# Kernel optimization log

Measured on AMD Instinct MI355X. Metric: run time of the kernel, lower is better.

The kernel has to match this reference:

```python
import jax, jax.numpy as jnp
import numpy as np

C = 3          # num_classes
A = 3          # num_anchors per cell
IMG = 1024.0
W_LOC, W_OBJ, W_CLS = 2.0, 1.0, 1.0
POS_T, NEG_T, HNM_RATIO = 0.5, 0.3, 3


def _make_anchors(H, W, stride):
    ys = (np.arange(H) + 0.5) * stride
    xs = (np.arange(W) + 0.5) * stride
    cy, cx = np.meshgrid(ys, xs, indexing='ij')
    sizes = np.array([2.0, 3.0, 4.0]) * stride          # A anchor scales
    cx = cx[:, :, None]; cy = cy[:, :, None]; s = sizes[None, None, :]
    a = np.stack([cx - s / 2, cy - s / 2, cx + s / 2, cy + s / 2], axis=-1)  # [H,W,A,4]
    return jnp.asarray(a.reshape(-1, 4), dtype=jnp.float32)


def setup_inputs() -> dict:
    key = jax.random.key(0)
    k1, k2, k3, k4, k5, k6 = jax.random.split(key, 6)
    B, M = 32, 20
    p1 = jax.random.normal(k1, (B, A * (5 + C), 128, 128), jnp.float32)
    p2 = jax.random.normal(k2, (B, A * (5 + C), 64, 64), jnp.float32)
    p3 = jax.random.normal(k3, (B, A * (5 + C), 32, 32), jnp.float32)
    anchors1 = _make_anchors(128, 128, 8)
    anchors2 = _make_anchors(64, 64, 16)
    anchors3 = _make_anchors(32, 32, 32)
    cxy = jax.random.uniform(k4, (B, M, 2), minval=0.0, maxval=IMG)
    wh = jax.random.uniform(k5, (B, M, 2), minval=16.0, maxval=256.0)
    boxes = jnp.clip(jnp.concatenate([cxy - wh / 2, cxy + wh / 2], -1), 0.0, IMG)
    labels = jax.random.randint(k6, (B, M), 0, C + 1)  # 0 = padding, 1..C = class
    return {"p1": p1, "p2": p2, "p3": p3,
            "anchors1": anchors1, "anchors2": anchors2, "anchors3": anchors3,
            "boxes": boxes, "labels": labels}


def _iou(anchors, boxes):
    # anchors [N,4], boxes [M,4], xyxy -> [N,M]
    lt = jnp.maximum(anchors[:, None, :2], boxes[None, :, :2])
    rb = jnp.minimum(anchors[:, None, 2:], boxes[None, :, 2:])
    wh = jnp.maximum(rb - lt, 0.0)
    inter = wh[..., 0] * wh[..., 1]
    area_a = (anchors[:, 2] - anchors[:, 0]) * (anchors[:, 3] - anchors[:, 1])
    area_b = (boxes[:, 2] - boxes[:, 0]) * (boxes[:, 3] - boxes[:, 1])
    return inter / jnp.maximum(area_a[:, None] + area_b[None, :] - inter, 1e-9)


def _decode(pred):
    # yolo_decode: [B, A*(5+C), H, W] -> deltas [B,N,4], obj [B,N], cls [B,N,C]; N = H*W*A
    B, _, H, W = pred.shape
    p = pred.reshape(B, A, 5 + C, H, W).transpose(0, 3, 4, 1, 2).reshape(B, H * W * A, 5 + C)
    return p[..., :4], p[..., 4], p[..., 5:]


def _level_loss(deltas, obj_logits, cls_logits, anchors, boxes, labels):
    # single image, single level
    valid = (labels > 0)
    iou = _iou(anchors, boxes) * valid[None, :].astype(deltas.dtype)
    best_iou = iou.max(axis=1)
    best_idx = iou.argmax(axis=1)
    pos = best_iou >= POS_T
    neg = best_iou < NEG_T
    mboxes = boxes[best_idx]
    mlabels = labels[best_idx]
    posf = pos.astype(deltas.dtype)
    # SmoothL1 (beta=1), mean over 4 coords, summed over positives
    d = jnp.abs(deltas - mboxes)
    sl1 = jnp.where(d < 1.0, 0.5 * d * d, d - 0.5).mean(axis=-1)
    loc = jnp.sum(sl1 * posf)
    # BCEWithLogits against objectness targets (= pos mask)
    x = obj_logits
    bce = jnp.maximum(x, 0.0) - x * posf + jnp.log1p(jnp.exp(-jnp.abs(x)))
    # hard negative mining on detached obj loss
    num_pos = pos.sum()
    num_neg = neg.sum()
    k = jnp.where(num_pos == 0,
                  jnp.minimum(100, num_neg),
                  jnp.minimum(num_pos * HNM_RATIO, num_neg))
    masked = jnp.where(neg, jax.lax.stop_gradient(bce), -1e9)
    order = jnp.argsort(-masked)
    ranks = jnp.zeros_like(order).at[order].set(jnp.arange(order.shape[0]))
    sel = (ranks < k) & neg
    obj = jnp.sum(bce * (pos | sel).astype(bce.dtype))
    # CrossEntropy over positives, labels shifted by -1
    logp = jax.nn.log_softmax(cls_logits, axis=-1)
    tgt = jnp.clip(mlabels - 1, 0, C - 1)
    nll = -jnp.take_along_axis(logp, tgt[:, None], axis=1)[:, 0]
    cls = jnp.sum(nll * posf)
    return loc, obj, cls, num_pos, sel.sum()


def reference(p1, p2, p3, anchors1, anchors2, anchors3, boxes, labels):
    total_loc = total_obj = total_cls = 0.0
    total_pos = total_neg = 0
    for pred, anchors in ((p1, anchors1), (p2, anchors2), (p3, anchors3)):
        deltas, obj_l, cls_l = _decode(pred)
        loc, obj, cls, npos, nneg = jax.vmap(
            _level_loss, in_axes=(0, 0, 0, None, 0, 0)
        )(deltas, obj_l, cls_l, anchors, boxes, labels)
        total_loc = total_loc + loc.sum()
        total_obj = total_obj + obj.sum()
        total_cls = total_cls + cls.sum()
        total_pos = total_pos + npos.sum()
        total_neg = total_neg + nneg.sum()
    norm = jnp.maximum(total_pos + total_neg, 1).astype(jnp.float32)
    loss_loc = W_LOC * total_loc / norm
    loss_obj = W_OBJ * total_obj / norm
    loss_cls = W_CLS * total_cls / jnp.maximum(total_pos, 1).astype(jnp.float32)
    return loss_loc + loss_obj + loss_cls, loss_loc, loss_obj, loss_cls
```

## Files before the change

### kernel.cpp

```cpp
#include <hip/hip_runtime.h>

#define NB 32
#define NM 20
#define NA 3
#define NCH 8
#define N0 49152
#define N1 12288
#define N2 3072


__device__ __forceinline__ float wredf(float v) {
  #pragma unroll
  for (int o = 32; o; o >>= 1) v += __shfl_down(v, o, 64);
  return v;
}

__device__ __forceinline__ float softplus_neg_abs(float x) {
  return __logf(1.0f + __expf(-fabsf(x)));
}

__device__ __forceinline__ float blockredf(float v, float* swred, int tid) {
  v = wredf(v);
  if ((tid & 63) == 0) swred[tid >> 6] = v;
  __syncthreads();
  float s = 0.f;
  if (tid == 0) {
    #pragma unroll
    for (int i = 0; i < 16; ++i) s += swred[i];
  }
  __syncthreads();
  return s;
}

__device__ __forceinline__ unsigned suffix1024(unsigned* scan, int tid) {
  #pragma unroll
  for (int d = 1; d < 1024; d <<= 1) {
    unsigned t = (tid + d < 1024) ? scan[tid + d] : 0u;
    __syncthreads();
    scan[tid] += t;
    __syncthreads();
  }
  return scan[tid];
}

__global__ __launch_bounds__(256, 8) void kA(
    const float* __restrict__ pr0, const float* __restrict__ pr1,
    const float* __restrict__ pr2,
    const float* __restrict__ boxes, const int* __restrict__ labels,
    unsigned* __restrict__ keys, float* __restrict__ partials)
{
  const int bx = blockIdx.x, b = blockIdx.y, tid = threadIdx.x;
  int blk, wshift, HW, nblk, koff, poff; float stride; const float* pred;
  if (bx < 64)      { blk = bx;      wshift = 7; HW = 16384; nblk = 64; koff = 0;            poff = 0;                         stride = 8.f;  pred = pr0; }
  else if (bx < 80) { blk = bx - 64; wshift = 6; HW = 4096;  nblk = 16; koff = NB * N0;      poff = NB * 64 * 5;               stride = 16.f; pred = pr1; }
  else              { blk = bx - 80; wshift = 5; HW = 1024;  nblk = 4;  koff = NB * (N0+N1); poff = NB * 64 * 5 + NB * 16 * 5; stride = 32.f; pred = pr2; }

  const int   nrows = 256 >> wshift;
  const int   h0    = blk * nrows;
  const float ymin  = ((float)h0 + 0.5f) * stride - 2.f * stride;
  const float ymax  = ((float)(h0 + nrows - 1) + 0.5f) * stride + 2.f * stride;

  __shared__ float4 sb4[NM + 1];
  __shared__ float2 sa2[NM + 1];
  __shared__ int    slab[NM + 1];
  __shared__ int    s_nv;
  if (tid < 64) {
    float x1 = 0, y1 = 0, x2 = 0, y2 = 0; int lb = 0; bool v = false;
    if (tid < NM) {
      x1 = boxes[(b * NM + tid) * 4 + 0];
      y1 = boxes[(b * NM + tid) * 4 + 1];
      x2 = boxes[(b * NM + tid) * 4 + 2];
      y2 = boxes[(b * NM + tid) * 4 + 3];
      lb = labels[b * NM + tid];
      v  = (lb > 0) && (y2 > ymin) && (y1 < ymax);
    }
    unsigned long long mask = __ballot(v);
    int pref = __popcll(mask & ((1ull << tid) - 1ull));
    if (v) {
      sb4[pref] = make_float4(x1, y1, x2, y2);
      sa2[pref] = make_float2((x2 - x1) * (y2 - y1), 0.f);
      slab[pref] = lb;
    }
    if (tid == 0) {
      int nv = (int)__popcll(mask);
      s_nv = nv;
      sb4[nv] = make_float4(0.f, 0.f, 0.f, 0.f);
      sa2[nv] = make_float2(0.f, 0.f);
    }
  }
  __syncthreads();

  const int hw = blk * 256 + tid;
  const int W  = 1 << wshift;
  const int w  = hw & (W - 1);
  const int h  = hw >> wshift;
  const float cx = ((float)w + 0.5f) * stride;
  const float cy = ((float)h + 0.5f) * stride;
  const float* pb = pred + (size_t)b * (NA * NCH) * HW + hw;

  float xo[NA];
  #pragma unroll
  for (int a = 0; a < NA; ++a) xo[a] = pb[(a * NCH + 4) * HW];

  float ax1[NA], ay1[NA], ax2[NA], ay2[NA], aar[NA];
  #pragma unroll
  for (int a = 0; a < NA; ++a) {
    const float s  = (2.0f + (float)a) * stride;
    const float hx = 0.5f * s;
    ax1[a] = cx - hx; ax2[a] = cx + hx;
    ay1[a] = cy - hx; ay2[a] = cy + hx;
    aar[a] = s * s;
  }

  float bi[NA] = {0.f, 0.f, 0.f};
  float bu[NA] = {1.f, 1.f, 1.f};
  int   bm[NA] = {0, 0, 0};
  const int nv = s_nv;

  float4 bb = sb4[0];
  float2 aa = sa2[0];
  for (int m = 0; m < nv; ++m) {
    const float4 nb = sb4[m + 1];
    const float2 na = sa2[m + 1];
    #pragma unroll
    for (int a = 0; a < NA; ++a) {
      float ix = fminf(ax2[a], bb.z) - fmaxf(ax1[a], bb.x);
      float iy = fminf(ay2[a], bb.w) - fmaxf(ay1[a], bb.y);
      float inter = fmaxf(ix, 0.f) * fmaxf(iy, 0.f);
      float un = (aar[a] + aa.x) - inter;
      bool better = inter * bu[a] > bi[a] * un;
      if (better) { bi[a] = inter; bu[a] = un; bm[a] = m; }
    }
    bb = nb; aa = na;
  }

  float loc_s = 0.f, obj_s = 0.f, cls_s = 0.f;
  float pos_c = 0.f, neg_c = 0.f;

  #pragma unroll
  for (int a = 0; a < NA; ++a) {
    const bool pos = 2.f * bi[a] >= bu[a];
    const bool neg = bi[a] < 0.3f * bu[a];
    const float x  = xo[a];
    const float sp = softplus_neg_abs(x);

    unsigned key = 0u;
    if (pos) {
      const int m = bm[a];
      pos_c += 1.f;
      obj_s += fmaxf(x, 0.f) - x + sp;
      const float4 tb = sb4[m];
      float ls = 0.f;
      float d0 = fabsf(pb[(a * NCH + 0) * HW] - tb.x);
      float d1 = fabsf(pb[(a * NCH + 1) * HW] - tb.y);
      float d2 = fabsf(pb[(a * NCH + 2) * HW] - tb.z);
      float d3 = fabsf(pb[(a * NCH + 3) * HW] - tb.w);
      ls += (d0 < 1.f) ? 0.5f * d0 * d0 : (d0 - 0.5f);
      ls += (d1 < 1.f) ? 0.5f * d1 * d1 : (d1 - 0.5f);
      ls += (d2 < 1.f) ? 0.5f * d2 * d2 : (d2 - 0.5f);
      ls += (d3 < 1.f) ? 0.5f * d3 * d3 : (d3 - 0.5f);
      loc_s += 0.25f * ls;
      float l0 = pb[(a * NCH + 5) * HW];
      float l1 = pb[(a * NCH + 6) * HW];
      float l2 = pb[(a * NCH + 7) * HW];
      float mx  = fmaxf(fmaxf(l0, l1), l2);
      float lse = mx + __logf(__expf(l0 - mx) + __expf(l1 - mx) + __expf(l2 - mx));
      int tgt = slab[m] - 1; tgt = tgt < 0 ? 0 : (tgt > 2 ? 2 : tgt);
      float lt = (tgt == 0) ? l0 : ((tgt == 1) ? l1 : l2);
      cls_s += lse - lt;
    } else if (neg) {
      neg_c += 1.f;
      float bn = fmaxf(x, 0.f) + sp;
      key = __float_as_uint(bn) | 0x80000000u;
    }
    keys[koff + b * (HW * NA) + a * HW + hw] = key;
  }

  loc_s = wredf(loc_s); obj_s = wredf(obj_s); cls_s = wredf(cls_s);
  pos_c = wredf(pos_c); neg_c = wredf(neg_c);
  __shared__ float sred[4][5];
  const int wv = tid >> 6;
  if ((tid & 63) == 0) {
    sred[wv][0] = loc_s; sred[wv][1] = obj_s; sred[wv][2] = cls_s;
    sred[wv][3] = pos_c; sred[wv][4] = neg_c;
  }
  __syncthreads();
  if (tid == 0) {
    float* slot = partials + poff + (size_t)(b * nblk + blk) * 5;
    #pragma unroll
    for (int j = 0; j < 5; ++j)
      slot[j] = sred[0][j] + sred[1][j] + sred[2][j] + sred[3][j];
  }
}

template<int NL4, bool GUARD>
__device__ float kb_core(const unsigned* __restrict__ kp, int n4, unsigned k,
                         unsigned* hist, unsigned* scan, float* fsum,
                         float* swred, unsigned* sh_sel, unsigned* sh_r, int tid)
{
  const uint4* kp4 = (const uint4*)kp;
  uint4 v[NL4];

  for (int i = tid; i < 4096; i += 1024) hist[i] = 0u;
  __syncthreads();

  #pragma unroll
  for (int j = 0; j < NL4; ++j)
    if (!GUARD || tid + j * 1024 < n4) v[j] = kp4[tid + j * 1024];

  #pragma unroll
  for (int j = 0; j < NL4; ++j)
    if (!GUARD || tid + j * 1024 < n4) {
      atomicAdd(&hist[v[j].x >> 20], 1u);
      atomicAdd(&hist[v[j].y >> 20], 1u);
      atomicAdd(&hist[v[j].z >> 20], 1u);
      atomicAdd(&hist[v[j].w >> 20], 1u);
    }
  __syncthreads();

  unsigned c0 = hist[tid*4], c1 = hist[tid*4+1], c2 = hist[tid*4+2], c3 = hist[tid*4+3];
  unsigned st = c0 + c1 + c2 + c3;
  scan[tid] = st;
  __syncthreads();
  unsigned I = suffix1024(scan, tid);
  unsigned H = I - st;
  if (H < k && k <= I) {
    unsigned cum = H;
    if (cum + c3 >= k)      { *sh_sel = tid*4+3; *sh_r = k - cum; }
    else { cum += c3;
      if (cum + c2 >= k)    { *sh_sel = tid*4+2; *sh_r = k - cum; }
      else { cum += c2;
        if (cum + c1 >= k)  { *sh_sel = tid*4+1; *sh_r = k - cum; }
        else { cum += c1;     *sh_sel = tid*4;   *sh_r = k - cum; } } }
  }
  __syncthreads();
  const unsigned pref0 = *sh_sel;
  const unsigned r1    = *sh_r;
  __syncthreads();

  hist[tid] = 0u; fsum[tid] = 0.f;
  __syncthreads();
  float s_above = 0.f;
  #pragma unroll
  for (int j = 0; j < NL4; ++j)
    if (!GUARD || tid + j * 1024 < n4) {
      #pragma unroll
      for (int cchan = 0; cchan < 4; ++cchan) {
        unsigned u = (&v[j].x)[cchan];
        unsigned d = u >> 20;
        float val = __uint_as_float(u & 0x7fffffffu);
        if (d > pref0) s_above += val;
        else if (d == pref0) {
          unsigned s2 = (u >> 10) & 1023u;
          atomicAdd(&hist[s2], 1u);
          atomicAdd(&fsum[s2], val);
        }
      }
    }
  __syncthreads();
  float S0 = blockredf(s_above, swred, tid);

  unsigned cc = hist[tid];
  scan[tid] = cc;
  __syncthreads();
  unsigned I1 = suffix1024(scan, tid);
  unsigned H1 = I1 - cc;
  if (H1 < r1 && r1 <= I1) { *sh_sel = tid; *sh_r = r1 - H1; }
  __syncthreads();
  const unsigned sel1 = *sh_sel;
  const unsigned r2   = *sh_r;
  float S1 = blockredf(tid > (int)sel1 ? fsum[tid] : 0.f, swred, tid);

  hist[tid] = 0u; fsum[tid] = 0.f;
  __syncthreads();
  const unsigned pref01 = (pref0 << 10) | sel1;
  #pragma unroll
  for (int j = 0; j < NL4; ++j)
    if (!GUARD || tid + j * 1024 < n4) {
      #pragma unroll
      for (int cchan = 0; cchan < 4; ++cchan) {
        unsigned u = (&v[j].x)[cchan];
        if ((u >> 10) == pref01) {
          unsigned s2 = u & 1023u;
          atomicAdd(&hist[s2], 1u);
          atomicAdd(&fsum[s2], __uint_as_float(u & 0x7fffffffu));
        }
      }
    }
  __syncthreads();

  cc = hist[tid];
  scan[tid] = cc;
  __syncthreads();
  unsigned I2 = suffix1024(scan, tid);
  unsigned H2 = I2 - cc;
  if (H2 < r2 && r2 <= I2) { *sh_sel = tid; *sh_r = r2 - H2; }
  __syncthreads();
  const unsigned sel2 = *sh_sel;
  const unsigned r3   = *sh_r;
  float S2 = blockredf(tid > (int)sel2 ? fsum[tid] : 0.f, swred, tid);

  const unsigned T = (pref01 << 10) | sel2;
  const float Tval = __uint_as_float(T & 0x7fffffffu);
  return S0 + S1 + S2 + Tval * (float)r3;
}

__global__ __launch_bounds__(1024) void kB(const unsigned* __restrict__ keys,
                                           const float* __restrict__ partials,
                                           float* __restrict__ finals)
{
  __shared__ unsigned hist[4096];
  __shared__ unsigned scan[1024];
  __shared__ float    fsum[1024];
  __shared__ float    swred[16];
  __shared__ float    gp[5];
  __shared__ unsigned sh_sel, sh_r;

  const int bl = blockIdx.x, lvl = bl / NB, b = bl % NB, tid = threadIdx.x;
  const int NLs[3]   = {N0, N1, N2};
  const int BASEs[3] = {0, NB * N0, NB * (N0 + N1)};
  const int NSL[3]   = {64, 16, 4};
  const int POFF[3]  = {0, NB * 64 * 5, NB * 64 * 5 + NB * 16 * 5};

  if (tid < 64) {
    float v0=0,v1=0,v2=0,v3=0,v4=0;
    if (tid < NSL[lvl]) {
      const float* pp = partials + POFF[lvl] + (size_t)(b * NSL[lvl] + tid) * 5;
      v0=pp[0]; v1=pp[1]; v2=pp[2]; v3=pp[3]; v4=pp[4];
    }
    v0=wredf(v0); v1=wredf(v1); v2=wredf(v2); v3=wredf(v3); v4=wredf(v4);
    if (tid==0){gp[0]=v0;gp[1]=v1;gp[2]=v2;gp[3]=v3;gp[4]=v4;}
  }
  __syncthreads();
  const int np = (int)gp[3], nn = (int)gp[4];
  const int k  = (np == 0) ? (nn < 100 ? nn : 100)
                           : (np * 3 < nn ? np * 3 : nn);

  float topk = 0.f;
  if (k > 0) {
    const unsigned* kp = keys + BASEs[lvl] + (size_t)b * NLs[lvl];
    if (lvl == 0)      topk = kb_core<12,false>(kp, 12288, (unsigned)k, hist, scan, fsum, swred, &sh_sel, &sh_r, tid);
    else if (lvl == 1) topk = kb_core<3, false>(kp, 3072,  (unsigned)k, hist, scan, fsum, swred, &sh_sel, &sh_r, tid);
    else               topk = kb_core<1, true >(kp, 768,   (unsigned)k, hist, scan, fsum, swred, &sh_sel, &sh_r, tid);
  }
  if (tid == 0) {
    float* f = finals + (size_t)bl * 5;
    f[0] = gp[0];
    f[1] = gp[1] + topk;
    f[2] = gp[2];
    f[3] = gp[3];
    f[4] = (float)k;
  }
}

__global__ void kC(const float* __restrict__ finals, float* __restrict__ out)
{
  const int tid = threadIdx.x;
  float loc = 0.f, obj = 0.f, cls = 0.f, pos = 0.f, sel = 0.f;
  if (tid < 96) {
    const float* f = finals + (size_t)tid * 5;
    loc = f[0]; obj = f[1]; cls = f[2]; pos = f[3]; sel = f[4];
  }
  loc = wredf(loc); obj = wredf(obj); cls = wredf(cls);
  pos = wredf(pos); sel = wredf(sel);
  __shared__ float sf[5][2];
  const int wv = tid >> 6;
  if ((tid & 63) == 0) { sf[0][wv] = loc; sf[1][wv] = obj; sf[2][wv] = cls;
                         sf[3][wv] = pos; sf[4][wv] = sel; }
  __syncthreads();
  if (tid == 0) {
    float L  = sf[0][0] + sf[0][1];
    float O  = sf[1][0] + sf[1][1];
    float Cl = sf[2][0] + sf[2][1];
    float P  = sf[3][0] + sf[3][1];
    float S  = sf[4][0] + sf[4][1];
    float norm  = fmaxf(P + S, 1.f);
    float l_loc = 2.0f * L / norm;
    float l_obj = O / norm;
    float l_cls = Cl / fmaxf(P, 1.f);
    out[0] = l_loc + l_obj + l_cls;
    out[1] = l_loc;
    out[2] = l_obj;
    out[3] = l_cls;
  }
}

extern "C" void kernel_launch(void* const* d_in, const int* in_sizes, int n_in,
                              void* d_out, int out_size, void* d_ws, size_t ws_size,
                              hipStream_t stream) {
  const float* p1     = (const float*)d_in[0];
  const float* p2     = (const float*)d_in[1];
  const float* p3     = (const float*)d_in[2];
  const float* boxes  = (const float*)d_in[6];
  const int*   labels = (const int*)d_in[7];
  float* out = (float*)d_out;

  char* ws = (char*)d_ws;
  float*    partials = (float*)ws;
  float*    finals   = (float*)(ws + 53760);
  unsigned* keys     = (unsigned*)(ws + 57344);

  kA<<<dim3(84, NB), 256, 0, stream>>>(p1, p2, p3, boxes, labels, keys, partials);
  kB<<<96, 1024, 0, stream>>>(keys, partials, finals);
  kC<<<1, 128, 0, stream>>>(finals, out);
}
```

Baseline: 37.89 us.

## Process four cells per thread, widen radix digits, wave-scan, fuse final reduce

kA now handles four consecutive grid cells per thread, using float4 objectness loads and uint4 key stores and sharing the y-overlap term across cells, so the grid shrinks from 84 to 21 blocks per image. The top-k radix select in kB moves to a 14-bit first digit with 9-bit refinement passes and replaces the barrier-heavy shared-memory suffix scan with a wavefront shuffle scan. The separate kC launch is removed: the last kB block, found through an atomic ticket, does the final reduction. The larger per-thread register footprint and fewer kA blocks may lower occupancy and latency hiding, and the 16K-entry histogram uses much more LDS per block.

```diff
diff --git a/kernel.cpp b/kernel.cpp
--- a/kernel.cpp
+++ b/kernel.cpp
@@ -32,36 +32,44 @@
   return s;
 }
 
-__device__ __forceinline__ unsigned suffix1024(unsigned* scan, int tid) {
-  #pragma unroll
-  for (int d = 1; d < 1024; d <<= 1) {
-    unsigned t = (tid + d < 1024) ? scan[tid + d] : 0u;
-    __syncthreads();
-    scan[tid] += t;
-    __syncthreads();
-  }
-  return scan[tid];
-}
-
-__global__ __launch_bounds__(256, 8) void kA(
+__device__ __forceinline__ unsigned suffix1024v(unsigned x, unsigned* swq, int tid) {
+  #pragma unroll
+  for (int o = 1; o < 64; o <<= 1) {
+    unsigned t = __shfl_down(x, o, 64);
+    if ((tid & 63) + o < 64) x += t;
+  }
+  unsigned wtot = __shfl(x, 0, 64);
+  __syncthreads();
+  if ((tid & 63) == 0) swq[tid >> 6] = wtot;
+  __syncthreads();
+  unsigned add = 0; const int wv = tid >> 6;
+  #pragma unroll
+  for (int i = 0; i < 16; ++i) add += (i > wv) ? swq[i] : 0u;
+  return x + add;
+}
+
+__global__ __launch_bounds__(256, 4) void kA(
     const float* __restrict__ pr0, const float* __restrict__ pr1,
     const float* __restrict__ pr2,
     const float* __restrict__ boxes, const int* __restrict__ labels,
-    unsigned* __restrict__ keys, float* __restrict__ partials)
+    unsigned* __restrict__ keys, float* __restrict__ partials,
+    int* __restrict__ ticket)
 {
   const int bx = blockIdx.x, b = blockIdx.y, tid = threadIdx.x;
   int blk, wshift, HW, nblk, koff, poff; float stride; const float* pred;
-  if (bx < 64)      { blk = bx;      wshift = 7; HW = 16384; nblk = 64; koff = 0;            poff = 0;                         stride = 8.f;  pred = pr0; }
-  else if (bx < 80) { blk = bx - 64; wshift = 6; HW = 4096;  nblk = 16; koff = NB * N0;      poff = NB * 64 * 5;               stride = 16.f; pred = pr1; }
-  else              { blk = bx - 80; wshift = 5; HW = 1024;  nblk = 4;  koff = NB * (N0+N1); poff = NB * 64 * 5 + NB * 16 * 5; stride = 32.f; pred = pr2; }
-
-  const int   nrows = 256 >> wshift;
+  if (bx < 16)      { blk = bx;      wshift = 7; HW = 16384; nblk = 16; koff = 0;            poff = 0;                       stride = 8.f;  pred = pr0; }
+  else if (bx < 20) { blk = bx - 16; wshift = 6; HW = 4096;  nblk = 4;  koff = NB * N0;      poff = NB * 16 * 5;             stride = 16.f; pred = pr1; }
+  else              { blk = 0;       wshift = 5; HW = 1024;  nblk = 1;  koff = NB * (N0+N1); poff = NB * 16 * 5 + NB * 4 * 5; stride = 32.f; pred = pr2; }
+
+  if (bx == 0 && b == 0 && tid == 0) *ticket = 0;
+
+  const int   nrows = 1024 >> wshift;
   const int   h0    = blk * nrows;
   const float ymin  = ((float)h0 + 0.5f) * stride - 2.f * stride;
   const float ymax  = ((float)(h0 + nrows - 1) + 0.5f) * stride + 2.f * stride;
 
   __shared__ float4 sb4[NM + 1];
-  __shared__ float2 sa2[NM + 1];
+  __shared__ float  sarea[NM + 1];
   __shared__ int    slab[NM + 1];
   __shared__ int    s_nv;
   if (tid < 64) {
@@ -78,103 +86,124 @@
     int pref = __popcll(mask & ((1ull << tid) - 1ull));
     if (v) {
       sb4[pref] = make_float4(x1, y1, x2, y2);
-      sa2[pref] = make_float2((x2 - x1) * (y2 - y1), 0.f);
+      sarea[pref] = (x2 - x1) * (y2 - y1);
       slab[pref] = lb;
     }
     if (tid == 0) {
       int nv = (int)__popcll(mask);
       s_nv = nv;
       sb4[nv] = make_float4(0.f, 0.f, 0.f, 0.f);
-      sa2[nv] = make_float2(0.f, 0.f);
-    }
-  }
-  __syncthreads();
-
-  const int hw = blk * 256 + tid;
-  const int W  = 1 << wshift;
-  const int w  = hw & (W - 1);
-  const int h  = hw >> wshift;
-  const float cx = ((float)w + 0.5f) * stride;
+      sarea[nv] = 0.f;
+    }
+  }
+  __syncthreads();
+
+  const int hw0 = blk * 1024 + tid * 4;
+  const int W   = 1 << wshift;
+  const int w0  = hw0 & (W - 1);
+  const int h   = hw0 >> wshift;
   const float cy = ((float)h + 0.5f) * stride;
-  const float* pb = pred + (size_t)b * (NA * NCH) * HW + hw;
-
-  float xo[NA];
-  #pragma unroll
-  for (int a = 0; a < NA; ++a) xo[a] = pb[(a * NCH + 4) * HW];
-
-  float ax1[NA], ay1[NA], ax2[NA], ay2[NA], aar[NA];
+  float cxe[4];
+  #pragma unroll
+  for (int e = 0; e < 4; ++e) cxe[e] = ((float)(w0 + e) + 0.5f) * stride;
+
+  const float* pb = pred + (size_t)b * (NA * NCH) * HW;
+
+  float xo[NA][4];
   #pragma unroll
   for (int a = 0; a < NA; ++a) {
-    const float s  = (2.0f + (float)a) * stride;
-    const float hx = 0.5f * s;
-    ax1[a] = cx - hx; ax2[a] = cx + hx;
-    ay1[a] = cy - hx; ay2[a] = cy + hx;
+    float4 o4 = *reinterpret_cast<const float4*>(pb + (a * NCH + 4) * HW + hw0);
+    xo[a][0] = o4.x; xo[a][1] = o4.y; xo[a][2] = o4.z; xo[a][3] = o4.w;
+  }
+
+  float hx[NA], aar[NA], ay1[NA], ay2[NA];
+  #pragma unroll
+  for (int a = 0; a < NA; ++a) {
+    const float s = (2.0f + (float)a) * stride;
+    hx[a]  = 0.5f * s;
     aar[a] = s * s;
-  }
-
-  float bi[NA] = {0.f, 0.f, 0.f};
-  float bu[NA] = {1.f, 1.f, 1.f};
-  int   bm[NA] = {0, 0, 0};
+    ay1[a] = cy - hx[a]; ay2[a] = cy + hx[a];
+  }
+
+  float bi[4][NA], bu[4][NA]; int bm[4][NA];
+  #pragma unroll
+  for (int e = 0; e < 4; ++e)
+    #pragma unroll
+    for (int a = 0; a < NA; ++a) { bi[e][a] = 0.f; bu[e][a] = 1.f; bm[e][a] = 0; }
+
   const int nv = s_nv;
-
   float4 bb = sb4[0];
-  float2 aa = sa2[0];
+  float  ba = sarea[0];
   for (int m = 0; m < nv; ++m) {
     const float4 nb = sb4[m + 1];
-    const float2 na = sa2[m + 1];
-    #pragma unroll
-    for (int a = 0; a < NA; ++a) {
-      float ix = fminf(ax2[a], bb.z) - fmaxf(ax1[a], bb.x);
-      float iy = fminf(ay2[a], bb.w) - fmaxf(ay1[a], bb.y);
-      float inter = fmaxf(ix, 0.f) * fmaxf(iy, 0.f);
-      float un = (aar[a] + aa.x) - inter;
-      bool better = inter * bu[a] > bi[a] * un;
-      if (better) { bi[a] = inter; bu[a] = un; bm[a] = m; }
-    }
-    bb = nb; aa = na;
+    const float  na = sarea[m + 1];
+    float iy[NA];
+    #pragma unroll
+    for (int a = 0; a < NA; ++a)
+      iy[a] = fmaxf(fminf(ay2[a], bb.w) - fmaxf(ay1[a], bb.y), 0.f);
+    #pragma unroll
+    for (int e = 0; e < 4; ++e) {
+      #pragma unroll
+      for (int a = 0; a < NA; ++a) {
+        float ix = fmaxf(fminf(cxe[e] + hx[a], bb.z) - fmaxf(cxe[e] - hx[a], bb.x), 0.f);
+        float inter = ix * iy[a];
+        float un = (aar[a] + ba) - inter;
+        bool better = inter * bu[e][a] > bi[e][a] * un;
+        if (better) { bi[e][a] = inter; bu[e][a] = un; bm[e][a] = m; }
+      }
+    }
+    bb = nb; ba = na;
   }
 
   float loc_s = 0.f, obj_s = 0.f, cls_s = 0.f;
   float pos_c = 0.f, neg_c = 0.f;
-
-  #pragma unroll
-  for (int a = 0; a < NA; ++a) {
-    const bool pos = 2.f * bi[a] >= bu[a];
-    const bool neg = bi[a] < 0.3f * bu[a];
-    const float x  = xo[a];
-    const float sp = softplus_neg_abs(x);
-
-    unsigned key = 0u;
-    if (pos) {
-      const int m = bm[a];
-      pos_c += 1.f;
-      obj_s += fmaxf(x, 0.f) - x + sp;
-      const float4 tb = sb4[m];
-      float ls = 0.f;
-      float d0 = fabsf(pb[(a * NCH + 0) * HW] - tb.x);
-      float d1 = fabsf(pb[(a * NCH + 1) * HW] - tb.y);
-      float d2 = fabsf(pb[(a * NCH + 2) * HW] - tb.z);
-      float d3 = fabsf(pb[(a * NCH + 3) * HW] - tb.w);
-      ls += (d0 < 1.f) ? 0.5f * d0 * d0 : (d0 - 0.5f);
-      ls += (d1 < 1.f) ? 0.5f * d1 * d1 : (d1 - 0.5f);
-      ls += (d2 < 1.f) ? 0.5f * d2 * d2 : (d2 - 0.5f);
-      ls += (d3 < 1.f) ? 0.5f * d3 * d3 : (d3 - 0.5f);
-      loc_s += 0.25f * ls;
-      float l0 = pb[(a * NCH + 5) * HW];
-      float l1 = pb[(a * NCH + 6) * HW];
-      float l2 = pb[(a * NCH + 7) * HW];
-      float mx  = fmaxf(fmaxf(l0, l1), l2);
-      float lse = mx + __logf(__expf(l0 - mx) + __expf(l1 - mx) + __expf(l2 - mx));
-      int tgt = slab[m] - 1; tgt = tgt < 0 ? 0 : (tgt > 2 ? 2 : tgt);
-      float lt = (tgt == 0) ? l0 : ((tgt == 1) ? l1 : l2);
-      cls_s += lse - lt;
-    } else if (neg) {
-      neg_c += 1.f;
-      float bn = fmaxf(x, 0.f) + sp;
-      key = __float_as_uint(bn) | 0x80000000u;
-    }
-    keys[koff + b * (HW * NA) + a * HW + hw] = key;
-  }
+  unsigned kk[NA][4];
+
+  #pragma unroll
+  for (int e = 0; e < 4; ++e) {
+    #pragma unroll
+    for (int a = 0; a < NA; ++a) {
+      const bool pos = 2.f * bi[e][a] >= bu[e][a];
+      const bool neg = bi[e][a] < 0.3f * bu[e][a];
+      const float x  = xo[a][e];
+      const float sp = softplus_neg_abs(x);
+
+      unsigned key = 0u;
+      if (pos) {
+        const int m = bm[e][a];
+        pos_c += 1.f;
+        obj_s += fmaxf(x, 0.f) - x + sp;
+        const float4 tb = sb4[m];
+        float d0 = fabsf(pb[(a * NCH + 0) * HW + hw0 + e] - tb.x);
+        float d1 = fabsf(pb[(a * NCH + 1) * HW + hw0 + e] - tb.y);
+        float d2 = fabsf(pb[(a * NCH + 2) * HW + hw0 + e] - tb.z);
+        float d3 = fabsf(pb[(a * NCH + 3) * HW + hw0 + e] - tb.w);
+        float ls = ((d0 < 1.f) ? 0.5f * d0 * d0 : (d0 - 0.5f))
+                 + ((d1 < 1.f) ? 0.5f * d1 * d1 : (d1 - 0.5f))
+                 + ((d2 < 1.f) ? 0.5f * d2 * d2 : (d2 - 0.5f))
+                 + ((d3 < 1.f) ? 0.5f * d3 * d3 : (d3 - 0.5f));
+        loc_s += 0.25f * ls;
+        float l0 = pb[(a * NCH + 5) * HW + hw0 + e];
+        float l1 = pb[(a * NCH + 6) * HW + hw0 + e];
+        float l2 = pb[(a * NCH + 7) * HW + hw0 + e];
+        float mx  = fmaxf(fmaxf(l0, l1), l2);
+        float lse = mx + __logf(__expf(l0 - mx) + __expf(l1 - mx) + __expf(l2 - mx));
+        int tgt = slab[m] - 1; tgt = tgt < 0 ? 0 : (tgt > 2 ? 2 : tgt);
+        float lt = (tgt == 0) ? l0 : ((tgt == 1) ? l1 : l2);
+        cls_s += lse - lt;
+      } else if (neg) {
+        neg_c += 1.f;
+        float bn = fmaxf(x, 0.f) + sp;
+        key = __float_as_uint(bn) | 0x80000000u;
+      }
+      kk[a][e] = key;
+    }
+  }
+
+  #pragma unroll
+  for (int a = 0; a < NA; ++a)
+    *reinterpret_cast<uint4*>(keys + koff + b * (HW * NA) + a * HW + hw0) =
+        make_uint4(kk[a][0], kk[a][1], kk[a][2], kk[a][3]);
 
   loc_s = wredf(loc_s); obj_s = wredf(obj_s); cls_s = wredf(cls_s);
   pos_c = wredf(pos_c); neg_c = wredf(neg_c);
@@ -195,13 +224,14 @@
 
 template<int NL4, bool GUARD>
 __device__ float kb_core(const unsigned* __restrict__ kp, int n4, unsigned k,
-                         unsigned* hist, unsigned* scan, float* fsum,
-                         float* swred, unsigned* sh_sel, unsigned* sh_r, int tid)
+                         unsigned* hist , float* fsum ,
+                         unsigned* swq, float* swred,
+                         unsigned* sh_sel, unsigned* sh_r, int tid)
 {
   const uint4* kp4 = (const uint4*)kp;
   uint4 v[NL4];
 
-  for (int i = tid; i < 4096; i += 1024) hist[i] = 0u;
+  for (int i = tid; i < 16384; i += 1024) hist[i] = 0u;
   __syncthreads();
 
   #pragma unroll
@@ -211,47 +241,46 @@
   #pragma unroll
   for (int j = 0; j < NL4; ++j)
     if (!GUARD || tid + j * 1024 < n4) {
-      atomicAdd(&hist[v[j].x >> 20], 1u);
-      atomicAdd(&hist[v[j].y >> 20], 1u);
-      atomicAdd(&hist[v[j].z >> 20], 1u);
-      atomicAdd(&hist[v[j].w >> 20], 1u);
-    }
-  __syncthreads();
-
-  unsigned c0 = hist[tid*4], c1 = hist[tid*4+1], c2 = hist[tid*4+2], c3 = hist[tid*4+3];
-  unsigned st = c0 + c1 + c2 + c3;
-  scan[tid] = st;
-  __syncthreads();
-  unsigned I = suffix1024(scan, tid);
+      atomicAdd(&hist[v[j].x >> 18], 1u);
+      atomicAdd(&hist[v[j].y >> 18], 1u);
+      atomicAdd(&hist[v[j].z >> 18], 1u);
+      atomicAdd(&hist[v[j].w >> 18], 1u);
+    }
+  __syncthreads();
+
+  unsigned st = 0;
+  #pragma unroll
+  for (int i = 0; i < 16; ++i) st += hist[tid * 16 + i];
+  unsigned I = suffix1024v(st, swq, tid);
   unsigned H = I - st;
   if (H < k && k <= I) {
-    unsigned cum = H;
-    if (cum + c3 >= k)      { *sh_sel = tid*4+3; *sh_r = k - cum; }
-    else { cum += c3;
-      if (cum + c2 >= k)    { *sh_sel = tid*4+2; *sh_r = k - cum; }
-      else { cum += c2;
-        if (cum + c1 >= k)  { *sh_sel = tid*4+1; *sh_r = k - cum; }
-        else { cum += c1;     *sh_sel = tid*4;   *sh_r = k - cum; } } }
+    unsigned cum = H; int selb = tid * 16; unsigned rr = 1;
+    for (int i = 15; i >= 0; --i) {
+      unsigned ci = hist[tid * 16 + i];
+      if (cum + ci >= k) { selb = tid * 16 + i; rr = k - cum; break; }
+      cum += ci;
+    }
+    *sh_sel = (unsigned)selb; *sh_r = rr;
   }
   __syncthreads();
   const unsigned pref0 = *sh_sel;
   const unsigned r1    = *sh_r;
   __syncthreads();
 
-  hist[tid] = 0u; fsum[tid] = 0.f;
+  if (tid < 512) { hist[tid] = 0u; fsum[tid] = 0.f; }
   __syncthreads();
   float s_above = 0.f;
   #pragma unroll
   for (int j = 0; j < NL4; ++j)
     if (!GUARD || tid + j * 1024 < n4) {
       #pragma unroll
-      for (int cchan = 0; cchan < 4; ++cchan) {
-        unsigned u = (&v[j].x)[cchan];
-        unsigned d = u >> 20;
+      for (int cc = 0; cc < 4; ++cc) {
+        unsigned u = (&v[j].x)[cc];
+        unsigned d = u >> 18;
         float val = __uint_as_float(u & 0x7fffffffu);
         if (d > pref0) s_above += val;
         else if (d == pref0) {
-          unsigned s2 = (u >> 10) & 1023u;
+          unsigned s2 = (u >> 9) & 511u;
           atomicAdd(&hist[s2], 1u);
           atomicAdd(&fsum[s2], val);
         }
@@ -260,67 +289,65 @@
   __syncthreads();
   float S0 = blockredf(s_above, swred, tid);
 
-  unsigned cc = hist[tid];
-  scan[tid] = cc;
-  __syncthreads();
-  unsigned I1 = suffix1024(scan, tid);
-  unsigned H1 = I1 - cc;
-  if (H1 < r1 && r1 <= I1) { *sh_sel = tid; *sh_r = r1 - H1; }
+  unsigned c1 = (tid < 512) ? hist[tid] : 0u;
+  unsigned I1 = suffix1024v(c1, swq, tid);
+  unsigned H1 = I1 - c1;
+  if (H1 < r1 && r1 <= I1) { *sh_sel = (unsigned)tid; *sh_r = r1 - H1; }
   __syncthreads();
   const unsigned sel1 = *sh_sel;
   const unsigned r2   = *sh_r;
-  float S1 = blockredf(tid > (int)sel1 ? fsum[tid] : 0.f, swred, tid);
-
-  hist[tid] = 0u; fsum[tid] = 0.f;
-  __syncthreads();
-  const unsigned pref01 = (pref0 << 10) | sel1;
+  float S1 = blockredf((tid < 512 && tid > (int)sel1) ? fsum[tid] : 0.f, swred, tid);
+
+  if (tid < 512) { hist[tid] = 0u; fsum[tid] = 0.f; }
+  __syncthreads();
+  const unsigned pref01 = (pref0 << 9) | sel1;
   #pragma unroll
   for (int j = 0; j < NL4; ++j)
     if (!GUARD || tid + j * 1024 < n4) {
       #pragma unroll
-      for (int cchan = 0; cchan < 4; ++cchan) {
-        unsigned u = (&v[j].x)[cchan];
-        if ((u >> 10) == pref01) {
-          unsigned s2 = u & 1023u;
-          atomicAdd(&hist[s2], 1u);
-          atomicAdd(&fsum[s2], __uint_as_float(u & 0x7fffffffu));
+      for (int cc = 0; cc < 4; ++cc) {
+        unsigned u = (&v[j].x)[cc];
+        if ((u >> 9) == pref01) {
+          atomicAdd(&hist[u & 511u], 1u);
+          atomicAdd(&fsum[u & 511u], __uint_as_float(u & 0x7fffffffu));
         }
       }
     }
   __syncthreads();
 
-  cc = hist[tid];
-  scan[tid] = cc;
-  __syncthreads();
-  unsigned I2 = suffix1024(scan, tid);
-  unsigned H2 = I2 - cc;
-  if (H2 < r2 && r2 <= I2) { *sh_sel = tid; *sh_r = r2 - H2; }
+  unsigned c2 = (tid < 512) ? hist[tid] : 0u;
+  unsigned I2 = suffix1024v(c2, swq, tid);
+  unsigned H2 = I2 - c2;
+  if (H2 < r2 && r2 <= I2) { *sh_sel = (unsigned)tid; *sh_r = r2 - H2; }
   __syncthreads();
   const unsigned sel2 = *sh_sel;
   const unsigned r3   = *sh_r;
-  float S2 = blockredf(tid > (int)sel2 ? fsum[tid] : 0.f, swred, tid);
-
-  const unsigned T = (pref01 << 10) | sel2;
+  float S2 = blockredf((tid < 512 && tid > (int)sel2) ? fsum[tid] : 0.f, swred, tid);
+
+  const unsigned T = (pref01 << 9) | sel2;
   const float Tval = __uint_as_float(T & 0x7fffffffu);
   return S0 + S1 + S2 + Tval * (float)r3;
 }
 
 __global__ __launch_bounds__(1024) void kB(const unsigned* __restrict__ keys,
                                            const float* __restrict__ partials,
-                                           float* __restrict__ finals)
+                                           float* __restrict__ finals,
+                                           int* __restrict__ ticket,
+                                           float* __restrict__ out)
 {
-  __shared__ unsigned hist[4096];
-  __shared__ unsigned scan[1024];
-  __shared__ float    fsum[1024];
+  __shared__ unsigned hist[16384];
+  __shared__ float    fsum[512];
+  __shared__ unsigned swq[16];
   __shared__ float    swred[16];
   __shared__ float    gp[5];
   __shared__ unsigned sh_sel, sh_r;
+  __shared__ int      s_last;
 
   const int bl = blockIdx.x, lvl = bl / NB, b = bl % NB, tid = threadIdx.x;
   const int NLs[3]   = {N0, N1, N2};
   const int BASEs[3] = {0, NB * N0, NB * (N0 + N1)};
-  const int NSL[3]   = {64, 16, 4};
-  const int POFF[3]  = {0, NB * 64 * 5, NB * 64 * 5 + NB * 16 * 5};
+  const int NSL[3]   = {16, 4, 1};
+  const int POFF[3]  = {0, NB * 16 * 5, NB * 16 * 5 + NB * 4 * 5};
 
   if (tid < 64) {
     float v0=0,v1=0,v2=0,v3=0,v4=0;
@@ -339,9 +366,9 @@
   float topk = 0.f;
   if (k > 0) {
     const unsigned* kp = keys + BASEs[lvl] + (size_t)b * NLs[lvl];
-    if (lvl == 0)      topk = kb_core<12,false>(kp, 12288, (unsigned)k, hist, scan, fsum, swred, &sh_sel, &sh_r, tid);
-    else if (lvl == 1) topk = kb_core<3, false>(kp, 3072,  (unsigned)k, hist, scan, fsum, swred, &sh_sel, &sh_r, tid);
-    else               topk = kb_core<1, true >(kp, 768,   (unsigned)k, hist, scan, fsum, swred, &sh_sel, &sh_r, tid);
+    if (lvl == 0)      topk = kb_core<12,false>(kp, 12288, (unsigned)k, hist, fsum, swq, swred, &sh_sel, &sh_r, tid);
+    else if (lvl == 1) topk = kb_core<3, false>(kp, 3072,  (unsigned)k, hist, fsum, swq, swred, &sh_sel, &sh_r, tid);
+    else               topk = kb_core<1, true >(kp, 768,   (unsigned)k, hist, fsum, swq, swred, &sh_sel, &sh_r, tid);
   }
   if (tid == 0) {
     float* f = finals + (size_t)bl * 5;
@@ -351,37 +378,35 @@
     f[3] = gp[3];
     f[4] = (float)k;
   }
-}
-
-__global__ void kC(const float* __restrict__ finals, float* __restrict__ out)
-{
-  const int tid = threadIdx.x;
-  float loc = 0.f, obj = 0.f, cls = 0.f, pos = 0.f, sel = 0.f;
-  if (tid < 96) {
-    const float* f = finals + (size_t)tid * 5;
-    loc = f[0]; obj = f[1]; cls = f[2]; pos = f[3]; sel = f[4];
-  }
-  loc = wredf(loc); obj = wredf(obj); cls = wredf(cls);
-  pos = wredf(pos); sel = wredf(sel);
-  __shared__ float sf[5][2];
-  const int wv = tid >> 6;
-  if ((tid & 63) == 0) { sf[0][wv] = loc; sf[1][wv] = obj; sf[2][wv] = cls;
-                         sf[3][wv] = pos; sf[4][wv] = sel; }
-  __syncthreads();
+
   if (tid == 0) {
-    float L  = sf[0][0] + sf[0][1];
-    float O  = sf[1][0] + sf[1][1];
-    float Cl = sf[2][0] + sf[2][1];
-    float P  = sf[3][0] + sf[3][1];
-    float S  = sf[4][0] + sf[4][1];
-    float norm  = fmaxf(P + S, 1.f);
-    float l_loc = 2.0f * L / norm;
-    float l_obj = O / norm;
-    float l_cls = Cl / fmaxf(P, 1.f);
-    out[0] = l_loc + l_obj + l_cls;
-    out[1] = l_loc;
-    out[2] = l_obj;
-    out[3] = l_cls;
+    __threadfence();
+    int t = atomicAdd(ticket, 1);
+    s_last = (t == 95) ? 1 : 0;
+  }
+  __syncthreads();
+  if (s_last) {
+    __threadfence();
+    float loc = 0.f, obj = 0.f, cls = 0.f, pos = 0.f, sel = 0.f;
+    if (tid < 96) {
+      const volatile float* f = finals + (size_t)tid * 5;
+      loc = f[0]; obj = f[1]; cls = f[2]; pos = f[3]; sel = f[4];
+    }
+    loc = blockredf(loc, swred, tid);
+    obj = blockredf(obj, swred, tid);
+    cls = blockredf(cls, swred, tid);
+    pos = blockredf(pos, swred, tid);
+    sel = blockredf(sel, swred, tid);
+    if (tid == 0) {
+      float norm  = fmaxf(pos + sel, 1.f);
+      float l_loc = 2.0f * loc / norm;
+      float l_obj = obj / norm;
+      float l_cls = cls / fmaxf(pos, 1.f);
+      out[0] = l_loc + l_obj + l_cls;
+      out[1] = l_loc;
+      out[2] = l_obj;
+      out[3] = l_cls;
+    }
   }
 }
 
@@ -398,9 +423,9 @@
   char* ws = (char*)d_ws;
   float*    partials = (float*)ws;
   float*    finals   = (float*)(ws + 53760);
+  int*      ticket   = (int*)(ws + 55680);
   unsigned* keys     = (unsigned*)(ws + 57344);
 
-  kA<<<dim3(84, NB), 256, 0, stream>>>(p1, p2, p3, boxes, labels, keys, partials);
-  kB<<<96, 1024, 0, stream>>>(keys, partials, finals);
-  kC<<<1, 128, 0, stream>>>(finals, out);
-}
+  kA<<<dim3(21, NB), 256, 0, stream>>>(p1, p2, p3, boxes, labels, keys, partials, ticket);
+  kB<<<96, 1024, 0, stream>>>(keys, partials, finals, ticket, out);
+}
```

Result: slower. 44.58 us (+17.6%).
